# Kernel tuning notes

Hardware: AMD Instinct MI355X
Metric: run time of the kernel (lower is better)

Reference implementation:

```python
import jax, jax.numpy as jnp
import numpy as np

B, T, D, H, L, R, V = 4, 1024, 1024, 16, 12, 32, 50257
HD = D // H
SCALING = 2.0   # lora_alpha(64) / lora_rank(32) at the default 16-bit precision
EPS = 1e-5
KV_QMAX = float(2 ** 8 - 1)  # kv_cache_bits = 8 (middle of [4,8,16])


def _ln(x, g, b):
    m = jnp.mean(x, -1, keepdims=True)
    v = jnp.mean(jnp.square(x - m), -1, keepdims=True)
    return (x - m) * jax.lax.rsqrt(v + EPS) * g + b


def _round_ste(x):
    return x + jax.lax.stop_gradient(jnp.round(x) - x)


def _fake_quant(x, mn, mx):
    # asymmetric learnable fake-quant with straight-through rounding
    scale = (mx - mn) / KV_QMAX
    zp = _round_ste(-mn / scale)
    q = jnp.clip(_round_ste(x / scale) + zp, 0.0, KV_QMAX)
    return (q - zp) * scale


def _sp_linear(x, w, b, la, lb):
    # quantized-base linear (full precision at 16-bit) + LoRA adapter (eval: no dropout)
    return x @ w + b + SCALING * ((x @ la) @ lb)


def setup_inputs() -> dict:
    key = jax.random.key(0)
    ks = iter(jax.random.split(key, 64))
    rn = lambda shape, s=0.02: jax.random.normal(next(ks), shape, jnp.float32) * s
    return {
        "input_ids": jax.random.randint(next(ks), (B, T), 0, V),
        "wte": rn((V, D)), "wpe": rn((T, D)),
        "ln1_g": jnp.ones((L, D)), "ln1_b": jnp.zeros((L, D)),
        "attn_w": rn((L, D, 3 * D)), "attn_b": jnp.zeros((L, 3 * D)),
        "attn_la": rn((L, D, R)), "attn_lb": rn((L, R, 3 * D)),
        "proj_w": rn((L, D, D)), "proj_b": jnp.zeros((L, D)),
        "proj_la": rn((L, D, R)), "proj_lb": rn((L, R, D)),
        "ln2_g": jnp.ones((L, D)), "ln2_b": jnp.zeros((L, D)),
        "fc_w": rn((L, D, 4 * D)), "fc_b": jnp.zeros((L, 4 * D)),
        "fc_la": rn((L, D, R)), "fc_lb": rn((L, R, 4 * D)),
        "mproj_w": rn((L, 4 * D, D)), "mproj_b": jnp.zeros((L, D)),
        "mproj_la": rn((L, 4 * D, R)), "mproj_lb": rn((L, R, D)),
        "kv_min": jnp.full((L,), -4.0), "kv_max": jnp.full((L,), 4.0),
        "lnf_g": jnp.ones((D,)), "lnf_b": jnp.zeros((D,)),
    }


def reference(input_ids, wte, wpe, ln1_g, ln1_b, attn_w, attn_b, attn_la, attn_lb,
              proj_w, proj_b, proj_la, proj_lb, ln2_g, ln2_b, fc_w, fc_b, fc_la,
              fc_lb, mproj_w, mproj_b, mproj_la, mproj_lb, kv_min, kv_max,
              lnf_g, lnf_b):
    mask = jnp.tril(jnp.ones((T, T), bool))
    h = wte[input_ids] + wpe[None, :T]  # [B,T,D] (dropout is identity in eval)

    def block(h, p):
        (g1, b1, aw, ab, ala, alb, pw, pb, pla, plb, g2, b2,
         fw, fb, fla, flb, mw, mb, mla, mlb, mn, mx) = p
        x = _ln(h, g1, b1)
        qkv = _sp_linear(x, aw, ab, ala, alb)  # [B,T,3D]
        q, k, v = jnp.split(qkv, 3, axis=-1)
        heads = lambda t: t.reshape(B, T, H, HD).transpose(0, 2, 1, 3)  # bhtd
        q, k, v = heads(q), heads(k), heads(v)
        # KV-cache fake quantization (default precision flag unset on attn)
        k = _fake_quant(k, mn, mx)
        v = _fake_quant(v, mn, mx)
        att = jnp.einsum('bhqd,bhkd->bhqk', q, k) / np.float32(np.sqrt(HD))
        att = jax.nn.softmax(jnp.where(mask, att, -jnp.inf), axis=-1)
        o = jnp.einsum('bhqk,bhkd->bhqd', att, v).transpose(0, 2, 1, 3).reshape(B, T, D)
        h = h + _sp_linear(o, pw, pb, pla, plb)
        x = _ln(h, g2, b2)
        m = jax.nn.gelu(_sp_linear(x, fw, fb, fla, flb), approximate=False)
        h = h + _sp_linear(m, mw, mb, mla, mlb)
        return h, None

    params = (ln1_g, ln1_b, attn_w, attn_b, attn_la, attn_lb, proj_w, proj_b,
              proj_la, proj_lb, ln2_g, ln2_b, fc_w, fc_b, fc_la, fc_lb,
              mproj_w, mproj_b, mproj_la, mproj_lb, kv_min, kv_max)
    h, _ = jax.lax.scan(block, h, params)
    return _ln(h, lnf_g, lnf_b)
```

## Files before the change

### kernel.cpp

```cpp
#include <hip/hip_runtime.h>
#include <hip/hip_bf16.h>


typedef __bf16 bf16x8 __attribute__((ext_vector_type(8)));
typedef float f32x4 __attribute__((ext_vector_type(4)));

static __device__ __forceinline__ float bf2f(unsigned short u) {
    union { unsigned int i; float f; } c; c.i = ((unsigned int)u) << 16; return c.f;
}
static __device__ __forceinline__ unsigned short f2bf(float f) {
    unsigned int u = __float_as_uint(f);
    u += 0x7fffu + ((u >> 16) & 1u);
    return (unsigned short)(u >> 16);
}

#define GL2LDS(g, l) __builtin_amdgcn_global_load_lds( \
    (const __attribute__((address_space(1))) unsigned int*)(g), \
    (__attribute__((address_space(3))) unsigned int*)(l), 16, 0, 0)

__global__ __launch_bounds__(256) void k_embed(const int* __restrict__ ids,
        const float* __restrict__ wte, const float* __restrict__ wpe,
        float* __restrict__ h) {
    int row = blockIdx.x;
    int t = row & 1023;
    int id = ids[row];
    int d = threadIdx.x * 4;
    float4 a = *(const float4*)(wte + (size_t)id * 1024 + d);
    float4 b = *(const float4*)(wpe + (size_t)t * 1024 + d);
    float4 o = make_float4(a.x + b.x, a.y + b.y, a.z + b.z, a.w + b.w);
    *(float4*)(h + (size_t)row * 1024 + d) = o;
}

template <bool BF16OUT>
__global__ __launch_bounds__(256) void k_ln(const float* __restrict__ h,
        const float* __restrict__ g, const float* __restrict__ be,
        unsigned short* __restrict__ xo, float* __restrict__ fo) {
    int row = blockIdx.x, tid = threadIdx.x;
    float4 v = *(const float4*)(h + (size_t)row * 1024 + tid * 4);
    float s = v.x + v.y + v.z + v.w;
    for (int off = 32; off; off >>= 1) s += __shfl_down(s, off);
    __shared__ float red[8];
    int wid = tid >> 6, lane = tid & 63;
    if (!lane) red[wid] = s;
    __syncthreads();
    float mean = (red[0] + red[1] + red[2] + red[3]) * (1.f / 1024.f);
    float dx = v.x - mean, dy = v.y - mean, dz = v.z - mean, dw = v.w - mean;
    float q = dx * dx + dy * dy + dz * dz + dw * dw;
    for (int off = 32; off; off >>= 1) q += __shfl_down(q, off);
    if (!lane) red[4 + wid] = q;
    __syncthreads();
    float var = (red[4] + red[5] + red[6] + red[7]) * (1.f / 1024.f);
    float inv = 1.0f / sqrtf(var + 1e-5f);
    float4 gv = *(const float4*)(g + tid * 4);
    float4 bv = *(const float4*)(be + tid * 4);
    float y0 = dx * inv * gv.x + bv.x;
    float y1 = dy * inv * gv.y + bv.y;
    float y2 = dz * inv * gv.z + bv.z;
    float y3 = dw * inv * gv.w + bv.w;
    if (BF16OUT) {
        ushort4 o;
        o.x = f2bf(y0); o.y = f2bf(y1); o.z = f2bf(y2); o.w = f2bf(y3);
        *(ushort4*)(xo + (size_t)row * 1024 + tid * 4) = o;
    } else {
        *(float4*)(fo + (size_t)row * 1024 + tid * 4) = make_float4(y0, y1, y2, y3);
    }
}

__global__ __launch_bounds__(256) void k_lora_mfma(const unsigned short* __restrict__ A,
        const unsigned short* __restrict__ laT, unsigned short* __restrict__ tmp, int K) {
    int rowBase = blockIdx.x * 16;
    int tid = threadIdx.x, w = tid >> 6, lane = tid & 63;
    int lrow = lane & 15, lk8 = (lane >> 4) * 8;
    int kq = K >> 2;
    f32x4 acc0 = {0.f, 0.f, 0.f, 0.f}, acc1 = {0.f, 0.f, 0.f, 0.f};
    const unsigned short* arow = A + (size_t)(rowBase + lrow) * K + w * kq + lk8;
    const unsigned short* b0p = laT + (size_t)lrow * K + w * kq + lk8;
    const unsigned short* b1p = laT + (size_t)(16 + lrow) * K + w * kq + lk8;
#pragma unroll 2
    for (int kt = 0; kt < kq; kt += 32) {
        bf16x8 af = *(const bf16x8*)(arow + kt);
        bf16x8 b0 = *(const bf16x8*)(b0p + kt);
        bf16x8 b1 = *(const bf16x8*)(b1p + kt);
        acc0 = __builtin_amdgcn_mfma_f32_16x16x32_bf16(af, b0, acc0, 0, 0, 0);
        acc1 = __builtin_amdgcn_mfma_f32_16x16x32_bf16(af, b1, acc1, 0, 0, 0);
    }
    __shared__ f32x4 red[2][4][64];
    red[0][w][lane] = acc0;
    red[1][w][lane] = acc1;
    __syncthreads();
    if (w == 0) {
        acc0 = red[0][0][lane] + red[0][1][lane] + red[0][2][lane] + red[0][3][lane];
        acc1 = red[1][0][lane] + red[1][1][lane] + red[1][2][lane] + red[1][3][lane];
        int lq = lane >> 4;
#pragma unroll
        for (int rg = 0; rg < 4; ++rg) {
            int row = rowBase + lq * 4 + rg;
            tmp[(size_t)row * 64 + lrow] = f2bf(acc0[rg]);
            tmp[(size_t)row * 64 + 16 + lrow] = f2bf(acc1[rg]);
            tmp[(size_t)row * 64 + 32 + lrow] = 0;
            tmp[(size_t)row * 64 + 48 + lrow] = 0;
        }
    }
}

__global__ __launch_bounds__(256) void k_prep(
        const float* awB, const float* pwB, const float* fwB, const float* mwB,
        const float* albB, const float* plbB, const float* flbB, const float* mlbB,
        const float* alaB, const float* plaB, const float* flaB, const float* mlaB,
        unsigned short* WTqB, unsigned short* WTpB, unsigned short* WTfB, unsigned short* WTmB,
        unsigned short* LTqB, unsigned short* LTpB, unsigned short* LTfB, unsigned short* LTmB,
        unsigned short* LAqB, unsigned short* LApB, unsigned short* LAfB, unsigned short* LAmB) {
    int bid = blockIdx.x;
    size_t l = blockIdx.y;
    const float* src; unsigned short* dst; int K, N, ntn, local, dstS; float scale = 1.f;
    if      (bid < 768)  { src = awB + l*3145728;  dst = WTqB + l*3145728; K = 1024; N = 3072; ntn = 48; local = bid; dstS = K; }
    else if (bid < 1024) { src = pwB + l*1048576;  dst = WTpB + l*1048576; K = 1024; N = 1024; ntn = 16; local = bid - 768; dstS = K; }
    else if (bid < 2048) { src = fwB + l*4194304;  dst = WTfB + l*4194304; K = 1024; N = 4096; ntn = 64; local = bid - 1024; dstS = K; }
    else if (bid < 3072) { src = mwB + l*4194304;  dst = WTmB + l*4194304; K = 4096; N = 1024; ntn = 16; local = bid - 2048; dstS = K; }
    else if (bid < 3120) { src = albB + l*98304;   dst = LTqB + l*196608;  K = 32;   N = 3072; ntn = 48; local = bid - 3072; scale = 2.f; dstS = 64; }
    else if (bid < 3136) { src = plbB + l*32768;   dst = LTpB + l*65536;   K = 32;   N = 1024; ntn = 16; local = bid - 3120; scale = 2.f; dstS = 64; }
    else if (bid < 3200) { src = flbB + l*131072;  dst = LTfB + l*262144;  K = 32;   N = 4096; ntn = 64; local = bid - 3136; scale = 2.f; dstS = 64; }
    else if (bid < 3216) { src = mlbB + l*32768;   dst = LTmB + l*65536;   K = 32;   N = 1024; ntn = 16; local = bid - 3200; scale = 2.f; dstS = 64; }
    else if (bid < 3232) { src = alaB + l*32768;   dst = LAqB + l*32768;   K = 1024; N = 32;   ntn = 1;  local = bid - 3216; dstS = K; }
    else if (bid < 3248) { src = plaB + l*32768;   dst = LApB + l*32768;   K = 1024; N = 32;   ntn = 1;  local = bid - 3232; dstS = K; }
    else if (bid < 3264) { src = flaB + l*32768;   dst = LAfB + l*32768;   K = 1024; N = 32;   ntn = 1;  local = bid - 3248; dstS = K; }
    else                 { src = mlaB + l*131072;  dst = LAmB + l*131072;  K = 4096; N = 32;   ntn = 1;  local = bid - 3264; dstS = K; }
    int kt = local / ntn, nt = local % ntn;
    int k0 = kt * 64, n0 = nt * 64;
    __shared__ unsigned short Tl[64][66];
    int tid = threadIdx.x;
    int c4 = (tid & 15) * 4;
#pragma unroll
    for (int p = 0; p < 4; ++p) {
        int kl = p * 16 + (tid >> 4);
        if (k0 + kl < K && n0 + c4 < N) {
            float4 v = *(const float4*)(src + (size_t)(k0 + kl) * N + n0 + c4);
            ushort2 o0, o1;
            o0.x = f2bf(v.x * scale); o0.y = f2bf(v.y * scale);
            o1.x = f2bf(v.z * scale); o1.y = f2bf(v.w * scale);
            *(ushort2*)&Tl[kl][c4] = o0;
            *(ushort2*)&Tl[kl][c4 + 2] = o1;
        }
    }
    __syncthreads();
    int nl = tid >> 2;
    int kc = (tid & 3) * 8;
    if (n0 + nl < N) {
#pragma unroll
        for (int hh = 0; hh < 2; ++hh) {
            int kb = kc + hh * 32;
            if (k0 + kb < K) {
                unsigned short pk[8];
#pragma unroll
                for (int j = 0; j < 8; ++j) {
                    pk[j] = Tl[kb + j][nl];
                }
                *(uint4*)(dst + (size_t)(n0 + nl) * dstS + k0 + kb) = *(const uint4*)pk;
            } else if (k0 + kb < dstS) {
                uint4 z; z.x = 0; z.y = 0; z.z = 0; z.w = 0;
                *(uint4*)(dst + (size_t)(n0 + nl) * dstS + k0 + kb) = z;
            }
        }
    }
}

template <int EPI>
__global__ __launch_bounds__(256) void k_gemm64(
        const unsigned short* __restrict__ A, const unsigned short* __restrict__ WT,
        const float* __restrict__ bias, const unsigned short* __restrict__ tmpA,
        const unsigned short* __restrict__ lbT, const float* __restrict__ res,
        float* __restrict__ outF, int N, int K) {
    __shared__ unsigned short Al[128 * 32];
    __shared__ unsigned short Bl[64 * 32];
    int tid = threadIdx.x;
    int nBase = blockIdx.x * 64, rowBase = blockIdx.y * 128;
    int w = tid >> 6, lane = tid & 63;
    int lrow = lane & 15, lk8 = (lane >> 4) * 8;
    int srow = lane >> 2;
    int scol = (lane & 3) * 8;
    f32x4 acc[2][4];
#pragma unroll
    for (int i = 0; i < 2; ++i)
#pragma unroll
        for (int j = 0; j < 4; ++j) acc[i][j] = f32x4{0.f, 0.f, 0.f, 0.f};
    int nk = K >> 5;
    for (int kt = 0; kt <= nk; ++kt) {
        bool mn = kt < nk;
        const unsigned short* sa[2];
        const unsigned short* sb;
#pragma unroll
        for (int i = 0; i < 2; ++i) {
            int r = rowBase + w * 32 + i * 16 + srow;
            sa[i] = mn ? A + (size_t)r * K + kt * 32 + scol
                       : tmpA + (size_t)r * 64 + scol;
        }
        {
            int r = nBase + w * 16 + srow;
            sb = mn ? WT + (size_t)r * K + kt * 32 + scol
                    : lbT + (size_t)r * 64 + scol;
        }
        __syncthreads();
#pragma unroll
        for (int i = 0; i < 2; ++i) GL2LDS(sa[i], &Al[(w * 32 + i * 16) * 32]);
        GL2LDS(sb, &Bl[(w * 16) * 32]);
        __syncthreads();
        bf16x8 af[2], bfr[4];
#pragma unroll
        for (int mt = 0; mt < 2; ++mt) af[mt] = *(const bf16x8*)&Al[(w * 32 + mt * 16 + lrow) * 32 + lk8];
#pragma unroll
        for (int nt = 0; nt < 4; ++nt) bfr[nt] = *(const bf16x8*)&Bl[(nt * 16 + lrow) * 32 + lk8];
#pragma unroll
        for (int mt = 0; mt < 2; ++mt)
#pragma unroll
            for (int nt = 0; nt < 4; ++nt)
                acc[mt][nt] = __builtin_amdgcn_mfma_f32_16x16x32_bf16(af[mt], bfr[nt], acc[mt][nt], 0, 0, 0);
    }
    int lq = lane >> 4;
#pragma unroll
    for (int nt = 0; nt < 4; ++nt) {
        int col = nBase + nt * 16 + lrow;
        float bv = bias[col];
#pragma unroll
        for (int mt = 0; mt < 2; ++mt) {
            int row0 = rowBase + w * 32 + mt * 16 + lq * 4;
#pragma unroll
            for (int rg = 0; rg < 4; ++rg) {
                int row = row0 + rg;
                float v = acc[mt][nt][rg] + bv;
                size_t idx = (size_t)row * N + col;
                if (EPI == 1) v += res[idx];
                outF[idx] = v;
            }
        }
    }
}

template <int EPI>
__global__ __launch_bounds__(512, 1) void k_gemm256(
        const unsigned short* __restrict__ A, const unsigned short* __restrict__ WT,
        const float* __restrict__ bias, const unsigned short* __restrict__ tmpA,
        const unsigned short* __restrict__ lbT,
        const float* __restrict__ kvmin, const float* __restrict__ kvmax, int layer,
        unsigned short* __restrict__ qh, unsigned short* __restrict__ kh,
        unsigned short* __restrict__ vh,
        float* __restrict__ outF, unsigned short* __restrict__ outH, int N, int K) {
    __shared__ unsigned short lds[9 * 8192];
    const int tid = threadIdx.x;
    const int wid = tid >> 6, lane = tid & 63;
    const int wr = wid >> 2, wc = wid & 3;
    const int nBase = blockIdx.x * 256, rowBase = blockIdx.y * 256;
    const int nk = (K >> 6) + 1;

    f32x4 acc[8][4];
#pragma unroll
    for (int i = 0; i < 8; ++i)
#pragma unroll
        for (int j = 0; j < 4; ++j) acc[i][j] = f32x4{0.f, 0.f, 0.f, 0.f};

    auto stage = [&](int s) {
        int kt = s >> 2, part = s & 3;
        bool dead = kt >= nk;
        unsigned short* dst = &lds[(dead ? 8 : (s & 7)) * 8192];
        bool isA = part >= 2;
        int half = part & 1;
        bool lora = (kt == nk - 1);
#pragma unroll
        for (int i = 0; i < 2; ++i) {
            int o = ((i * 8 + wid) << 10) + (lane << 4);
            int r = o >> 7;
            int col = ((o & 127) ^ (((o >> 9) & 3) << 5)) >> 1;
            const unsigned short* src;
            if (dead) {
                src = A + (lane << 3);
            } else if (isA) {
                int grow = rowBase + half * 128 + r;
                src = lora ? tmpA + (size_t)grow * 64 + col
                           : A + (size_t)grow * K + kt * 64 + col;
            } else {
                int gcol = nBase + half * 128 + r;
                src = lora ? lbT + (size_t)gcol * 64 + col
                           : WT + (size_t)gcol * K + kt * 64 + col;
            }
            GL2LDS(src, dst + ((i * 8 + wid) << 9));
        }
    };

    stage(0); stage(1); stage(2); stage(3);
    stage(4); stage(5); stage(6);
    asm volatile("s_waitcnt vmcnt(6)" ::: "memory");
    __builtin_amdgcn_s_barrier();

    for (int kt = 0; kt < nk; ++kt) {
        const unsigned short* aPart = &lds[(((kt & 1) << 2) + 2 + wr) * 8192];
        const unsigned short* bPart = &lds[(((kt & 1) << 2) + (wc >> 1)) * 8192];
        bf16x8 bfr[4][2];
#pragma unroll
        for (int p = 0; p < 4; ++p) {
            bf16x8 af[2][2];
#pragma unroll
            for (int mm = 0; mm < 2; ++mm)
#pragma unroll
                for (int kk = 0; kk < 2; ++kk) {
                    int row = (p * 2 + mm) * 16 + (lane & 15);
                    int cb = (kk * 64 + ((lane >> 4) << 4)) ^ (((row >> 2) & 3) << 5);
                    af[mm][kk] = *(const bf16x8*)&aPart[row * 64 + (cb >> 1)];
                }
            if (p == 0) {
#pragma unroll
                for (int n = 0; n < 4; ++n)
#pragma unroll
                    for (int kk = 0; kk < 2; ++kk) {
                        int row = ((wc & 1) << 6) + n * 16 + (lane & 15);
                        int cb = (kk * 64 + ((lane >> 4) << 4)) ^ (((row >> 2) & 3) << 5);
                        bfr[n][kk] = *(const bf16x8*)&bPart[row * 64 + (cb >> 1)];
                    }
            }
            stage(p == 0 ? 4 * (kt + 1) + 3 : 4 * (kt + 2) + (p - 1));
            __builtin_amdgcn_s_barrier();
            __builtin_amdgcn_s_setprio(1);
#pragma unroll
            for (int mm = 0; mm < 2; ++mm)
#pragma unroll
                for (int n = 0; n < 4; ++n)
#pragma unroll
                    for (int kk = 0; kk < 2; ++kk)
                        acc[p * 2 + mm][n] = __builtin_amdgcn_mfma_f32_16x16x32_bf16(
                            af[mm][kk], bfr[n][kk], acc[p * 2 + mm][n], 0, 0, 0);
            __builtin_amdgcn_s_setprio(0);
            if (p == 3) asm volatile("s_waitcnt vmcnt(6)" ::: "memory");
            __builtin_amdgcn_s_barrier();
        }
    }

    if (EPI == 3) {
        const int b = rowBase >> 10, t0 = rowBase & 1023;
        const int sec = nBase >> 10, nb = nBase & 1023;
        const int lrow = lane & 15, lq4 = (lane >> 4) << 2;
        float qs = 1.f, qzp = 0.f, qinv = 1.f;
        if (sec) {
            float mnv = kvmin[layer], mxv = kvmax[layer];
            qs = (mxv - mnv) * (1.f / 255.f);
            qzp = rintf(-mnv / qs);
            qinv = 1.f / qs;
        }
#pragma unroll
        for (int n = 0; n < 4; ++n) {
            int dd = wc * 64 + n * 16 + lrow;
            float bv = bias[nBase + dd];
#pragma unroll
            for (int m = 0; m < 8; ++m) {
#pragma unroll
                for (int rg = 0; rg < 4; ++rg) {
                    int tt = wr * 128 + m * 16 + lq4 + rg;
                    float v = acc[m][n][rg] + bv;
                    if (sec) {
                        float qv = rintf(v * qinv) + qzp;
                        qv = fminf(fmaxf(qv, 0.f), 255.f);
                        v = (qv - qzp) * qs;
                    }
                    int r = (sec == 2) ? dd : tt;
                    int c = (sec == 2) ? tt : dd;
                    lds[r * 256 + (c ^ ((r & 7) << 3))] = f2bf(v);
                }
            }
        }
        __syncthreads();
        if (sec < 2) {
            unsigned short* dstp = sec ? kh : qh;
            int tL = tid & 255;
            int hp = tid >> 8;
#pragma unroll
            for (int hi = 0; hi < 2; ++hi) {
                int dL = (hp * 2 + hi) * 64;
                int hh = (nb >> 6) + hp * 2 + hi;
                size_t base = (((size_t)(b * 16 + hh)) * 1024 + t0 + tL) * 64;
#pragma unroll
                for (int j = 0; j < 8; ++j) {
                    int c = (dL + j * 8) ^ ((tL & 7) << 3);
                    *(uint4*)(dstp + base + j * 8) = *(const uint4*)&lds[tL * 256 + c];
                }
            }
        } else {
            int dL = tid & 255;
            int th = (tid >> 8) * 128;
            int hh = (nb >> 6) + (dL >> 6);
            size_t base = (((size_t)(b * 16 + hh)) * 64 + (dL & 63)) * 1024 + t0 + th;
#pragma unroll
            for (int j = 0; j < 16; ++j) {
                int c = (th + j * 8) ^ ((dL & 7) << 3);
                *(uint4*)(vh + base + j * 8) = *(const uint4*)&lds[dL * 256 + c];
            }
        }
    } else {
#pragma unroll
        for (int n = 0; n < 4; ++n) {
            int col = nBase + wc * 64 + n * 16 + (lane & 15);
            float bv = bias[col];
#pragma unroll
            for (int m = 0; m < 8; ++m) {
                int row0 = rowBase + wr * 128 + m * 16 + ((lane >> 4) << 2);
#pragma unroll
                for (int rg = 0; rg < 4; ++rg) {
                    int row = row0 + rg;
                    float v = acc[m][n][rg] + bv;
                    size_t idx = (size_t)row * N + col;
                    if (EPI == 2) {
                        v = 0.5f * v * (1.f + erff(v * 0.70710678118654752f));
                        outH[idx] = f2bf(v);
                    } else {
                        outF[idx] = v;
                    }
                }
            }
        }
    }
}

__global__ __launch_bounds__(256) void k_attn(const unsigned short* __restrict__ qh,
        const unsigned short* __restrict__ kh, const unsigned short* __restrict__ vh,
        unsigned short* __restrict__ o) {
    int fid = blockIdx.y * 16 + blockIdx.x;
    int wgid = (fid & 7) * 128 + (fid >> 3);
    int bh = wgid >> 4, qb = wgid & 15;
    int b = bh >> 4, hh = bh & 15;
    int tid = threadIdx.x, w = tid >> 6, lane = tid & 63;
    int cq = lane & 15;
    int g = lane >> 4;
    int lk8 = g * 8;
    __shared__ unsigned short Kl[64][72];
    __shared__ unsigned short Vt[64][72];
    __shared__ unsigned short Pl[4][16][72];
    const float SCL = 0.18033688011112042f;
    int qrow = qb * 64 + w * 16 + cq;
    bf16x8 aq[2];
    aq[0] = *(const bf16x8*)(qh + ((size_t)bh * 1024 + qrow) * 64 + lk8);
    aq[1] = *(const bf16x8*)(qh + ((size_t)bh * 1024 + qrow) * 64 + 32 + lk8);
    f32x4 od[4];
#pragma unroll
    for (int i = 0; i < 4; ++i) od[i] = f32x4{0.f, 0.f, 0.f, 0.f};
    float mrun = -3e38f, lrun = 0.f;
    int rl = tid >> 2, seg = (tid & 3) * 16;
    for (int kb = 0; kb <= qb; ++kb) {
        __syncthreads();
        {
            size_t kbase = ((size_t)bh * 1024 + kb * 64 + rl) * 64 + seg;
            *(uint4*)&Kl[rl][seg] = *(const uint4*)(kh + kbase);
            *(uint4*)&Kl[rl][seg + 8] = *(const uint4*)(kh + kbase + 8);
            size_t vbase = ((size_t)bh * 64 + rl) * 1024 + kb * 64 + seg;
            *(uint4*)&Vt[rl][seg] = *(const uint4*)(vh + vbase);
            *(uint4*)&Vt[rl][seg + 8] = *(const uint4*)(vh + vbase + 8);
        }
        __syncthreads();
        f32x4 st[4];
#pragma unroll
        for (int ktile = 0; ktile < 4; ++ktile) {
            f32x4 sacc = f32x4{0.f, 0.f, 0.f, 0.f};
#pragma unroll
            for (int dh = 0; dh < 2; ++dh) {
                bf16x8 bk = *(const bf16x8*)&Kl[ktile * 16 + cq][dh * 32 + lk8];
                sacc = __builtin_amdgcn_mfma_f32_16x16x32_bf16(bk, aq[dh], sacc, 0, 0, 0);
            }
            st[ktile] = sacc * SCL;
        }
        if (kb == qb) {
#pragma unroll
            for (int ktile = 0; ktile < 4; ++ktile) {
#pragma unroll
                for (int rg = 0; rg < 4; ++rg) {
                    int kidx = kb * 64 + ktile * 16 + g * 4 + rg;
                    if (kidx > qrow) st[ktile][rg] = -3e38f;
                }
            }
        }
        float pmax = st[0][0];
#pragma unroll
        for (int ktile = 0; ktile < 4; ++ktile)
#pragma unroll
            for (int rg = 0; rg < 4; ++rg) pmax = fmaxf(pmax, st[ktile][rg]);
        pmax = fmaxf(pmax, __shfl_xor(pmax, 16));
        pmax = fmaxf(pmax, __shfl_xor(pmax, 32));
        float mnew = fmaxf(mrun, pmax);
        float sum = 0.f;
#pragma unroll
        for (int ktile = 0; ktile < 4; ++ktile)
#pragma unroll
            for (int rg = 0; rg < 4; ++rg) {
                st[ktile][rg] = exp2f(st[ktile][rg] - mnew);
                sum += st[ktile][rg];
            }
        sum += __shfl_xor(sum, 16);
        sum += __shfl_xor(sum, 32);
        float corr = exp2f(mrun - mnew);
        lrun = lrun * corr + sum;
        mrun = mnew;
#pragma unroll
        for (int rg = 0; rg < 4; ++rg) {
            float cv = __shfl(corr, (lane & 48) | (g * 4 + rg));
#pragma unroll
            for (int dt = 0; dt < 4; ++dt) od[dt][rg] *= cv;
        }
#pragma unroll
        for (int ktile = 0; ktile < 4; ++ktile) {
            ushort4 pw;
            pw.x = f2bf(st[ktile][0]); pw.y = f2bf(st[ktile][1]);
            pw.z = f2bf(st[ktile][2]); pw.w = f2bf(st[ktile][3]);
            *(ushort4*)&Pl[w][cq][ktile * 16 + g * 4] = pw;
        }
        bf16x8 pa[2];
        pa[0] = *(const bf16x8*)&Pl[w][cq][lk8];
        pa[1] = *(const bf16x8*)&Pl[w][cq][32 + lk8];
#pragma unroll
        for (int dt = 0; dt < 4; ++dt) {
#pragma unroll
            for (int kh2 = 0; kh2 < 2; ++kh2) {
                bf16x8 bv = *(const bf16x8*)&Vt[dt * 16 + cq][kh2 * 32 + lk8];
                od[dt] = __builtin_amdgcn_mfma_f32_16x16x32_bf16(pa[kh2], bv, od[dt], 0, 0, 0);
            }
        }
    }
#pragma unroll
    for (int rg = 0; rg < 4; ++rg) {
        float lv = __shfl(lrun, (lane & 48) | (g * 4 + rg));
        float inv = 1.0f / lv;
        int row = qb * 64 + w * 16 + g * 4 + rg;
#pragma unroll
        for (int dt = 0; dt < 4; ++dt) {
            float val = od[dt][rg] * inv;
            o[((size_t)(b * 1024 + row)) * 1024 + hh * 64 + dt * 16 + cq] = f2bf(val);
        }
    }
}

extern "C" void kernel_launch(void* const* d_in, const int* in_sizes, int n_in,
                              void* d_out, int out_size, void* d_ws, size_t ws_size,
                              hipStream_t stream) {
    const int*   ids      = (const int*)d_in[0];
    const float* wte      = (const float*)d_in[1];
    const float* wpe      = (const float*)d_in[2];
    const float* ln1_g    = (const float*)d_in[3];
    const float* ln1_b    = (const float*)d_in[4];
    const float* attn_w   = (const float*)d_in[5];
    const float* attn_b   = (const float*)d_in[6];
    const float* attn_la  = (const float*)d_in[7];
    const float* attn_lb  = (const float*)d_in[8];
    const float* proj_w   = (const float*)d_in[9];
    const float* proj_b   = (const float*)d_in[10];
    const float* proj_la  = (const float*)d_in[11];
    const float* proj_lb  = (const float*)d_in[12];
    const float* ln2_g    = (const float*)d_in[13];
    const float* ln2_b    = (const float*)d_in[14];
    const float* fc_w     = (const float*)d_in[15];
    const float* fc_b     = (const float*)d_in[16];
    const float* fc_la    = (const float*)d_in[17];
    const float* fc_lb    = (const float*)d_in[18];
    const float* mproj_w  = (const float*)d_in[19];
    const float* mproj_b  = (const float*)d_in[20];
    const float* mproj_la = (const float*)d_in[21];
    const float* mproj_lb = (const float*)d_in[22];
    const float* kv_min   = (const float*)d_in[23];
    const float* kv_max   = (const float*)d_in[24];
    const float* lnf_g    = (const float*)d_in[25];
    const float* lnf_b    = (const float*)d_in[26];

    char* ws = (char*)d_ws;
    size_t off = 0;
    auto alloc = [&](size_t bytes) -> char* {
        char* p = ws + off;
        off = (off + bytes + 255) & ~(size_t)255;
        return p;
    };
    float*          h   = (float*)alloc(4096ull * 1024 * 4);
    unsigned short* xb  = (unsigned short*)alloc(4096ull * 1024 * 2);
    unsigned short* tmp = (unsigned short*)alloc(4096ull * 64 * 2);
    unsigned short* qhb = (unsigned short*)alloc(64ull * 1024 * 64 * 2);
    unsigned short* khb = (unsigned short*)alloc(64ull * 1024 * 64 * 2);
    unsigned short* vhb = (unsigned short*)alloc(64ull * 64 * 1024 * 2);
    unsigned short* ob  = (unsigned short*)alloc(4096ull * 1024 * 2);
    unsigned short* mb  = (unsigned short*)alloc(4096ull * 4096 * 2);
    unsigned short* WTq = (unsigned short*)alloc(12ull * 3072 * 1024 * 2);
    unsigned short* WTp = (unsigned short*)alloc(12ull * 1024 * 1024 * 2);
    unsigned short* WTf = (unsigned short*)alloc(12ull * 4096 * 1024 * 2);
    unsigned short* WTm = (unsigned short*)alloc(12ull * 1024 * 4096 * 2);
    unsigned short* LTq = (unsigned short*)alloc(12ull * 3072 * 64 * 2);
    unsigned short* LTp = (unsigned short*)alloc(12ull * 1024 * 64 * 2);
    unsigned short* LTf = (unsigned short*)alloc(12ull * 4096 * 64 * 2);
    unsigned short* LTm = (unsigned short*)alloc(12ull * 1024 * 64 * 2);
    unsigned short* LAq = (unsigned short*)alloc(12ull * 32 * 1024 * 2);
    unsigned short* LAp = (unsigned short*)alloc(12ull * 32 * 1024 * 2);
    unsigned short* LAf = (unsigned short*)alloc(12ull * 32 * 1024 * 2);
    unsigned short* LAm = (unsigned short*)alloc(12ull * 32 * 4096 * 2);

    k_embed<<<4096, 256, 0, stream>>>(ids, wte, wpe, h);
    k_prep<<<dim3(3328, 12), 256, 0, stream>>>(
        attn_w, proj_w, fc_w, mproj_w,
        attn_lb, proj_lb, fc_lb, mproj_lb,
        attn_la, proj_la, fc_la, mproj_la,
        WTq, WTp, WTf, WTm, LTq, LTp, LTf, LTm, LAq, LAp, LAf, LAm);
    for (int l = 0; l < 12; ++l) {
        k_ln<true><<<4096, 256, 0, stream>>>(h, ln1_g + l * 1024, ln1_b + l * 1024, xb, nullptr);
        k_lora_mfma<<<256, 256, 0, stream>>>(xb, LAq + (size_t)l * 32768, tmp, 1024);
        k_gemm256<3><<<dim3(12, 16), 512, 0, stream>>>(xb, WTq + (size_t)l * 3145728,
                                                       attn_b + l * 3072, tmp, LTq + (size_t)l * 196608,
                                                       kv_min, kv_max, l, qhb, khb, vhb,
                                                       nullptr, nullptr, 3072, 1024);
        k_attn<<<dim3(16, 64), 256, 0, stream>>>(qhb, khb, vhb, ob);
        k_lora_mfma<<<256, 256, 0, stream>>>(ob, LAp + (size_t)l * 32768, tmp, 1024);
        k_gemm64<1><<<dim3(16, 32), 256, 0, stream>>>(ob, WTp + (size_t)l * 1048576,
                                                      proj_b + l * 1024, tmp, LTp + (size_t)l * 65536,
                                                      h, h, 1024, 1024);
        k_ln<true><<<4096, 256, 0, stream>>>(h, ln2_g + l * 1024, ln2_b + l * 1024, xb, nullptr);
        k_lora_mfma<<<256, 256, 0, stream>>>(xb, LAf + (size_t)l * 32768, tmp, 1024);
        k_gemm256<2><<<dim3(16, 16), 512, 0, stream>>>(xb, WTf + (size_t)l * 4194304,
                                                       fc_b + l * 4096, tmp, LTf + (size_t)l * 262144,
                                                       nullptr, nullptr, 0, nullptr, nullptr, nullptr,
                                                       nullptr, mb, 4096, 1024);
        k_lora_mfma<<<256, 256, 0, stream>>>(mb, LAm + (size_t)l * 131072, tmp, 4096);
        k_gemm64<1><<<dim3(16, 32), 256, 0, stream>>>(mb, WTm + (size_t)l * 4194304,
                                                      mproj_b + l * 1024, tmp, LTm + (size_t)l * 65536,
                                                      h, h, 1024, 4096);
    }
    k_ln<false><<<4096, 256, 0, stream>>>(h, lnf_g, lnf_b, nullptr, (float*)d_out);
}
```

Measured before the change: 4.094 ms.

## Replace 128x64 projection GEMM with pipelined 128x128 swizzled-LDS kernel

Replaces the simple single-buffered 128x64 GEMM used for the attention output and MLP down projections with a 128x128 tile kernel. The new kernel uses K=64 steps, a multi-stage global-to-LDS prefetch pipeline with vmcnt waits, an XOR-swizzled LDS layout against bank conflicts, and raised wave priority around the MFMA blocks. The goal is to hide memory latency and increase data reuse per tile. In exchange the launch has half as many blocks (256 on a large GPU), so occupancy is lower and some CUs may sit idle.

New measurement: 3.624 ms. -11.5%, faster.

```diff
diff --git a/kernel.cpp b/kernel.cpp
--- a/kernel.cpp
+++ b/kernel.cpp
@@ -165,68 +165,106 @@
 }
 
 template <int EPI>
-__global__ __launch_bounds__(256) void k_gemm64(
+__global__ __launch_bounds__(256, 1) void k_gemm128(
         const unsigned short* __restrict__ A, const unsigned short* __restrict__ WT,
         const float* __restrict__ bias, const unsigned short* __restrict__ tmpA,
         const unsigned short* __restrict__ lbT, const float* __restrict__ res,
         float* __restrict__ outF, int N, int K) {
-    __shared__ unsigned short Al[128 * 32];
-    __shared__ unsigned short Bl[64 * 32];
-    int tid = threadIdx.x;
-    int nBase = blockIdx.x * 64, rowBase = blockIdx.y * 128;
-    int w = tid >> 6, lane = tid & 63;
-    int lrow = lane & 15, lk8 = (lane >> 4) * 8;
-    int srow = lane >> 2;
-    int scol = (lane & 3) * 8;
-    f32x4 acc[2][4];
-#pragma unroll
-    for (int i = 0; i < 2; ++i)
+    __shared__ unsigned short lds[9 * 4096];
+    const int tid = threadIdx.x;
+    const int wid = tid >> 6, lane = tid & 63;
+    const int wr = wid >> 1, wc = wid & 1;
+    const int nBase = blockIdx.x * 128, rowBase = blockIdx.y * 128;
+    const int nk = (K >> 6) + 1;
+
+    f32x4 acc[4][4];
+#pragma unroll
+    for (int i = 0; i < 4; ++i)
 #pragma unroll
         for (int j = 0; j < 4; ++j) acc[i][j] = f32x4{0.f, 0.f, 0.f, 0.f};
-    int nk = K >> 5;
-    for (int kt = 0; kt <= nk; ++kt) {
-        bool mn = kt < nk;
-        const unsigned short* sa[2];
-        const unsigned short* sb;
+
+    auto stage = [&](int s) {
+        int kt = s >> 2, part = s & 3;
+        bool dead = kt >= nk;
+        unsigned short* dst = &lds[(dead ? 8 : (s & 7)) * 4096];
+        bool isA = part >= 2;
+        int half = part & 1;
+        bool lora = (kt == nk - 1);
 #pragma unroll
         for (int i = 0; i < 2; ++i) {
-            int r = rowBase + w * 32 + i * 16 + srow;
-            sa[i] = mn ? A + (size_t)r * K + kt * 32 + scol
-                       : tmpA + (size_t)r * 64 + scol;
-        }
-        {
-            int r = nBase + w * 16 + srow;
-            sb = mn ? WT + (size_t)r * K + kt * 32 + scol
-                    : lbT + (size_t)r * 64 + scol;
-        }
-        __syncthreads();
-#pragma unroll
-        for (int i = 0; i < 2; ++i) GL2LDS(sa[i], &Al[(w * 32 + i * 16) * 32]);
-        GL2LDS(sb, &Bl[(w * 16) * 32]);
-        __syncthreads();
-        bf16x8 af[2], bfr[4];
-#pragma unroll
-        for (int mt = 0; mt < 2; ++mt) af[mt] = *(const bf16x8*)&Al[(w * 32 + mt * 16 + lrow) * 32 + lk8];
-#pragma unroll
-        for (int nt = 0; nt < 4; ++nt) bfr[nt] = *(const bf16x8*)&Bl[(nt * 16 + lrow) * 32 + lk8];
-#pragma unroll
-        for (int mt = 0; mt < 2; ++mt)
-#pragma unroll
-            for (int nt = 0; nt < 4; ++nt)
-                acc[mt][nt] = __builtin_amdgcn_mfma_f32_16x16x32_bf16(af[mt], bfr[nt], acc[mt][nt], 0, 0, 0);
-    }
-    int lq = lane >> 4;
-#pragma unroll
-    for (int nt = 0; nt < 4; ++nt) {
-        int col = nBase + nt * 16 + lrow;
+            int o = ((i * 4 + wid) << 10) + (lane << 4);
+            int r = o >> 7;
+            int col = ((o & 127) ^ (((o >> 9) & 3) << 5)) >> 1;
+            const unsigned short* src;
+            if (dead) {
+                src = A + (lane << 3);
+            } else if (isA) {
+                int grow = rowBase + half * 64 + r;
+                src = lora ? tmpA + (size_t)grow * 64 + col
+                           : A + (size_t)grow * K + kt * 64 + col;
+            } else {
+                int gcol = nBase + half * 64 + r;
+                src = lora ? lbT + (size_t)gcol * 64 + col
+                           : WT + (size_t)gcol * K + kt * 64 + col;
+            }
+            GL2LDS(src, dst + ((i * 4 + wid) << 9));
+        }
+    };
+
+    stage(0); stage(1); stage(2); stage(3);
+    stage(4); stage(5); stage(6);
+    asm volatile("s_waitcnt vmcnt(6)" ::: "memory");
+    __builtin_amdgcn_s_barrier();
+
+    for (int kt = 0; kt < nk; ++kt) {
+        const unsigned short* aPart = &lds[(((kt & 1) << 2) + 2 + wr) * 4096];
+        const unsigned short* bPart = &lds[(((kt & 1) << 2) + wc) * 4096];
+        bf16x8 bfr[4][2];
+#pragma unroll
+        for (int p = 0; p < 4; ++p) {
+            bf16x8 af[2];
+#pragma unroll
+            for (int kk = 0; kk < 2; ++kk) {
+                int row = p * 16 + (lane & 15);
+                int cb = (kk * 64 + ((lane >> 4) << 4)) ^ (((row >> 2) & 3) << 5);
+                af[kk] = *(const bf16x8*)&aPart[row * 64 + (cb >> 1)];
+            }
+            if (p == 0) {
+#pragma unroll
+                for (int n = 0; n < 4; ++n)
+#pragma unroll
+                    for (int kk = 0; kk < 2; ++kk) {
+                        int row = n * 16 + (lane & 15);
+                        int cb = (kk * 64 + ((lane >> 4) << 4)) ^ (((row >> 2) & 3) << 5);
+                        bfr[n][kk] = *(const bf16x8*)&bPart[row * 64 + (cb >> 1)];
+                    }
+            }
+            stage(p == 0 ? 4 * (kt + 1) + 3 : 4 * (kt + 2) + (p - 1));
+            __builtin_amdgcn_s_barrier();
+            __builtin_amdgcn_s_setprio(1);
+#pragma unroll
+            for (int n = 0; n < 4; ++n)
+#pragma unroll
+                for (int kk = 0; kk < 2; ++kk)
+                    acc[p][n] = __builtin_amdgcn_mfma_f32_16x16x32_bf16(
+                        af[kk], bfr[n][kk], acc[p][n], 0, 0, 0);
+            __builtin_amdgcn_s_setprio(0);
+            if (p == 3) asm volatile("s_waitcnt vmcnt(6)" ::: "memory");
+            __builtin_amdgcn_s_barrier();
+        }
+    }
+
+#pragma unroll
+    for (int n = 0; n < 4; ++n) {
+        int col = nBase + wc * 64 + n * 16 + (lane & 15);
         float bv = bias[col];
 #pragma unroll
-        for (int mt = 0; mt < 2; ++mt) {
-            int row0 = rowBase + w * 32 + mt * 16 + lq * 4;
+        for (int m = 0; m < 4; ++m) {
+            int row0 = rowBase + wr * 64 + m * 16 + ((lane >> 4) << 2);
 #pragma unroll
             for (int rg = 0; rg < 4; ++rg) {
                 int row = row0 + rg;
-                float v = acc[mt][nt][rg] + bv;
+                float v = acc[m][n][rg] + bv;
                 size_t idx = (size_t)row * N + col;
                 if (EPI == 1) v += res[idx];
                 outF[idx] = v;
@@ -605,7 +643,7 @@
                                                        nullptr, nullptr, 3072, 1024);
         k_attn<<<dim3(16, 64), 256, 0, stream>>>(qhb, khb, vhb, ob);
         k_lora_mfma<<<256, 256, 0, stream>>>(ob, LAp + (size_t)l * 32768, tmp, 1024);
-        k_gemm64<1><<<dim3(16, 32), 256, 0, stream>>>(ob, WTp + (size_t)l * 1048576,
+        k_gemm128<1><<<dim3(8, 32), 256, 0, stream>>>(ob, WTp + (size_t)l * 1048576,
                                                       proj_b + l * 1024, tmp, LTp + (size_t)l * 65536,
                                                       h, h, 1024, 1024);
         k_ln<true><<<4096, 256, 0, stream>>>(h, ln2_g + l * 1024, ln2_b + l * 1024, xb, nullptr);
@@ -615,7 +653,7 @@
                                                        nullptr, nullptr, 0, nullptr, nullptr, nullptr,
                                                        nullptr, mb, 4096, 1024);
         k_lora_mfma<<<256, 256, 0, stream>>>(mb, LAm + (size_t)l * 131072, tmp, 4096);
-        k_gemm64<1><<<dim3(16, 32), 256, 0, stream>>>(mb, WTm + (size_t)l * 4194304,
+        k_gemm128<1><<<dim3(8, 32), 256, 0, stream>>>(mb, WTm + (size_t)l * 4194304,
                                                       mproj_b + l * 1024, tmp, LTm + (size_t)l * 65536,
                                                       h, h, 1024, 4096);
     }
```
